# Performance work log

Hardware: AMD Instinct MI355X
Metric: run time of the kernel (lower is better)

The kernel has to match this reference:

```python
import jax, jax.numpy as jnp
import numpy as np

B, T, D, UNITS = 32, 2048, 512, 512


def setup_inputs() -> dict:
    key = jax.random.key(0)
    ks = jax.random.split(key, 8)
    s_d = 1.0 / np.sqrt(D)
    s_u = 1.0 / np.sqrt(UNITS)
    return {
        "features": jax.random.normal(ks[0], (B, T, D), jnp.float32),
        "hidden": jax.random.normal(ks[1], (B, D), jnp.float32),
        "W1": jax.random.normal(ks[2], (D, UNITS), jnp.float32) * s_d,
        "b1": jnp.zeros((UNITS,), jnp.float32),
        "W2": jax.random.normal(ks[3], (D, UNITS), jnp.float32) * s_d,
        "b2": jnp.zeros((UNITS,), jnp.float32),
        "V": jax.random.normal(ks[4], (UNITS, 1), jnp.float32) * s_u,
        "bv": jnp.zeros((1,), jnp.float32),
    }


def reference(features, hidden, W1, b1, W2, b2, V, bv):
    # features: [B,T,D], hidden: [B,D]
    proj_f = jnp.einsum('btd,du->btu', features, W1) + b1      # [B,T,U]
    proj_h = (hidden @ W2 + b2)[:, None, :]                    # [B,1,U]
    score = jnp.tanh(proj_f + proj_h)                          # [B,T,U]
    logits = jnp.einsum('btu,uo->bto', score, V) + bv          # [B,T,1]
    attn = jax.nn.softmax(logits, axis=1)                      # softmax over time
    context = jnp.sum(attn * features, axis=1)                 # [B,D]
    return context, attn
```

## Files before the change

### kernel.cpp

```cpp
#include <hip/hip_runtime.h>
#include <hip/hip_bf16.h>

typedef __bf16 bf16x8 __attribute__((ext_vector_type(8)));
typedef float  float4v __attribute__((ext_vector_type(4)));
typedef unsigned short u16;
typedef u16 u16x8 __attribute__((ext_vector_type(8)));

#define NB 32
#define NT 2048
#define ND 512
#define NU 512
#define BK 64

__device__ __forceinline__ u16 f2bf(float f) {
    union { float f; unsigned u; } v; v.f = f;
    unsigned u = v.u;
    return (u16)((u + 0x7fffu + ((u >> 16) & 1u)) >> 16);
}

__device__ __forceinline__ u16x8 cvt8(float4v a, float4v b) {
    union { __hip_bfloat162 h[4]; u16x8 v; } u;
    u.h[0] = __float22bfloat162_rn(make_float2(a[0], a[1]));
    u.h[1] = __float22bfloat162_rn(make_float2(a[2], a[3]));
    u.h[2] = __float22bfloat162_rn(make_float2(b[0], b[1]));
    u.h[3] = __float22bfloat162_rn(make_float2(b[2], b[3]));
    return u.v;
}

__device__ __forceinline__ float fast_tanh(float x) {
    float e = __expf(-2.f * x);
    return 2.f / (1.f + e) - 1.f;
}

__global__ void k_setup(const float* __restrict__ W1, u16* __restrict__ w1t,
                        const float* __restrict__ hidden, const float* __restrict__ W2,
                        const float* __restrict__ b2, float* __restrict__ projh,
                        float* __restrict__ ctx) {
    __shared__ u16 tile[32][33];
    __shared__ float h[ND];
    __shared__ float part[4][64];
    if (threadIdx.x < 32) ctx[blockIdx.x * 32 + threadIdx.x] = 0.f;

    if (blockIdx.x < 256) {
        int bd = (blockIdx.x & 15) * 32;
        int bu = (blockIdx.x >> 4) * 32;
        int tx = threadIdx.x & 31, ty = threadIdx.x >> 5;
        #pragma unroll
        for (int i = 0; i < 4; ++i)
            tile[ty + i * 8][tx] = f2bf(W1[(bd + ty + i * 8) * NU + bu + tx]);
        __syncthreads();
        #pragma unroll
        for (int i = 0; i < 4; ++i)
            w1t[(bu + ty + i * 8) * ND + bd + tx] = tile[tx][ty + i * 8];
    } else {
        int blk = blockIdx.x - 256;
        int b  = blk >> 3;
        int uc = (blk & 7) * 64;
        int ui = threadIdx.x & 63;
        int du = threadIdx.x >> 6;
        for (int i = threadIdx.x; i < ND; i += 256) h[i] = hidden[b * ND + i];
        __syncthreads();
        int u = uc + ui;
        float acc = 0.f;
        int d0 = du * 128;
        #pragma unroll 8
        for (int d = 0; d < 128; ++d) acc += h[d0 + d] * W2[(d0 + d) * NU + u];
        part[du][ui] = acc;
        __syncthreads();
        if (threadIdx.x < 64)
            projh[b * NU + u] = part[0][ui] + part[1][ui] + part[2][ui] + part[3][ui] + b2[u];
    }
}

__global__ __launch_bounds__(512, 4)
void k_logits(const float* __restrict__ feat, const u16* __restrict__ w1t,
              const float* __restrict__ b1, const float* __restrict__ projh,
              const float* __restrict__ V, float* __restrict__ logits) {
    __shared__ __align__(16) u16 aT[64 * BK];
    __shared__ __align__(16) u16 bT[512 * BK];

    const int row0 = blockIdx.x * 64;
    const int b    = row0 >> 11;
    const int tid  = threadIdx.x;
    const int wave = tid >> 6, lane = tid & 63;
    const int quad = lane >> 4, col = lane & 15;

    float4v acc[4][4];
    #pragma unroll
    for (int mt = 0; mt < 4; ++mt)
        #pragma unroll
        for (int nt = 0; nt < 4; ++nt) acc[mt][nt] = (float4v)0.f;

    const int r_a = tid >> 3, c_a = tid & 7;
    const int wc_a = c_a ^ (r_a & 7);
    const float* agp = feat + (long)row0 * ND + r_a * ND + c_a * 8;

    float4v f0 = *(const float4v*)agp;
    float4v f1 = *(const float4v*)(agp + 4);

    for (int p = 0; p < 8; ++p) {
        const int k0 = p * BK;
        #pragma unroll
        for (int j = 0; j < 8; ++j) {
            int s  = j * 512 + tid;
            int r  = s >> 3;
            int gc = (s & 7) ^ (r & 7);
            const u16* gp = w1t + r * ND + k0 + gc * 8;
            u16* lp = &bT[(j * 512 + wave * 64) * 8];
            __builtin_amdgcn_global_load_lds(
                (const __attribute__((address_space(1))) unsigned int*)gp,
                (__attribute__((address_space(3))) unsigned int*)lp, 16, 0, 0);
        }
        *(u16x8*)(&aT[r_a * BK + wc_a * 8]) = cvt8(f0, f1);
        __syncthreads();
        if (p < 7) {
            const float* gp = agp + (p + 1) * BK;
            f0 = *(const float4v*)gp;
            f1 = *(const float4v*)(gp + 4);
        }
        #pragma unroll
        for (int ks = 0; ks < 2; ++ks) {
            bf16x8 af[4], bf[4];
            #pragma unroll
            for (int mt = 0; mt < 4; ++mt) {
                int ra = mt * 16 + col;
                af[mt] = *(const bf16x8*)(&aT[ra * BK + (((ks * 4 + quad) ^ (ra & 7)) * 8)]);
            }
            #pragma unroll
            for (int nt = 0; nt < 4; ++nt) {
                int rb = wave * 64 + nt * 16 + col;
                bf[nt] = *(const bf16x8*)(&bT[rb * BK + (((ks * 4 + quad) ^ (rb & 7)) * 8)]);
            }
            #pragma unroll
            for (int nt = 0; nt < 4; ++nt)
                #pragma unroll
                for (int mt = 0; mt < 4; ++mt)
                    acc[mt][nt] = __builtin_amdgcn_mfma_f32_16x16x32_bf16(af[mt], bf[nt], acc[mt][nt], 0, 0, 0);
        }
        __syncthreads();
    }

    float b1v[4], phv[4], Vv[4];
    #pragma unroll
    for (int nt = 0; nt < 4; ++nt) {
        int u = wave * 64 + nt * 16 + col;
        b1v[nt] = b1[u];
        phv[nt] = projh[b * NU + u];
        Vv[nt]  = V[u];
    }
    float (*partial)[64] = (float(*)[64])aT;
    #pragma unroll
    for (int mt = 0; mt < 4; ++mt) {
        #pragma unroll
        for (int rg = 0; rg < 4; ++rg) {
            float s = 0.f;
            #pragma unroll
            for (int nt = 0; nt < 4; ++nt) {
                float pv = acc[mt][nt][rg] + b1v[nt] + phv[nt];
                s += fast_tanh(pv) * Vv[nt];
            }
            s += __shfl_xor(s, 1);
            s += __shfl_xor(s, 2);
            s += __shfl_xor(s, 4);
            s += __shfl_xor(s, 8);
            if (col == 0) partial[wave][mt * 16 + quad * 4 + rg] = s;
        }
    }
    __syncthreads();
    if (tid < 64) {
        float v = 0.f;
        #pragma unroll
        for (int w = 0; w < 8; ++w) v += partial[w][tid];
        logits[row0 + tid] = v;
    }
}

__global__ __launch_bounds__(256)
void k_ctxsm(const float* __restrict__ feat, const float* __restrict__ logits,
             float* __restrict__ attn, float* __restrict__ ctx) {
    __shared__ float wm[4], ws[4];
    __shared__ float als[64];
    __shared__ float4v part[128];
    const int b  = blockIdx.x >> 5;
    const int tc = blockIdx.x & 31;
    const int t0 = tc * 64;
    const int tid = threadIdx.x;
    const int lane = tid & 63, wave = tid >> 6;
    const float* lg = logits + b * NT;

    float4v l0 = *(const float4v*)(lg + tid * 8);
    float4v l1 = *(const float4v*)(lg + tid * 8 + 4);
    float m = fmaxf(fmaxf(fmaxf(l0[0], l0[1]), fmaxf(l0[2], l0[3])),
                    fmaxf(fmaxf(l1[0], l1[1]), fmaxf(l1[2], l1[3])));
    for (int o = 1; o < 64; o <<= 1) m = fmaxf(m, __shfl_xor(m, o));
    if (lane == 0) wm[wave] = m;
    __syncthreads();
    m = fmaxf(fmaxf(wm[0], wm[1]), fmaxf(wm[2], wm[3]));
    float s = 0.f;
    #pragma unroll
    for (int i = 0; i < 4; ++i) s += __expf(l0[i] - m);
    #pragma unroll
    for (int i = 0; i < 4; ++i) s += __expf(l1[i] - m);
    for (int o = 1; o < 64; o <<= 1) s += __shfl_xor(s, o);
    if (lane == 0) ws[wave] = s;
    __syncthreads();
    const float inv = 1.f / (ws[0] + ws[1] + ws[2] + ws[3]);

    if (tid < 64) {
        float a = __expf(lg[t0 + tid] - m) * inv;
        als[tid] = a;
        attn[b * NT + t0 + tid] = a;
    }
    __syncthreads();

    const int di = tid & 127, tg = tid >> 7;
    const float* fb = feat + ((long)b * NT + t0 + tg * 32) * ND + di * 4;
    float4v acc = (float4v)0.f;
    #pragma unroll 8
    for (int t = 0; t < 32; ++t) {
        float a = als[tg * 32 + t];
        float4v fv = *(const float4v*)(fb + (long)t * ND);
        acc += a * fv;
    }
    if (tg) part[di] = acc;
    __syncthreads();
    if (!tg) {
        acc += part[di];
        float* cp = &ctx[b * ND + di * 4];
        atomicAdd(cp + 0, acc[0]);
        atomicAdd(cp + 1, acc[1]);
        atomicAdd(cp + 2, acc[2]);
        atomicAdd(cp + 3, acc[3]);
    }
}

extern "C" void kernel_launch(void* const* d_in, const int* in_sizes, int n_in,
                              void* d_out, int out_size, void* d_ws, size_t ws_size,
                              hipStream_t stream) {
    const float* feat   = (const float*)d_in[0];
    const float* hidden = (const float*)d_in[1];
    const float* W1     = (const float*)d_in[2];
    const float* b1     = (const float*)d_in[3];
    const float* W2     = (const float*)d_in[4];
    const float* b2     = (const float*)d_in[5];
    const float* V      = (const float*)d_in[6];

    float* out_ctx  = (float*)d_out;
    float* out_attn = (float*)d_out + NB * ND;

    u16*   w1t    = (u16*)d_ws;
    float* projh  = (float*)((char*)d_ws + 512 * 1024);
    float* logits = (float*)((char*)d_ws + 512 * 1024 + 64 * 1024);

    k_setup <<<512, 256, 0, stream>>>(W1, w1t, hidden, W2, b2, projh, out_ctx);
    k_logits<<<1024, 512, 0, stream>>>(feat, w1t, b1, projh, V, logits);
    k_ctxsm <<<1024, 256, 0, stream>>>(feat, logits, out_attn, out_ctx);
}
```

Measured before the change: 259.0 us.

## Fuse softmax-weighted context into logits kernel using unnormalized exp sums

```diff
diff --git a/kernel.cpp b/kernel.cpp
--- a/kernel.cpp
+++ b/kernel.cpp
@@ -35,11 +35,13 @@
 __global__ void k_setup(const float* __restrict__ W1, u16* __restrict__ w1t,
                         const float* __restrict__ hidden, const float* __restrict__ W2,
                         const float* __restrict__ b2, float* __restrict__ projh,
-                        float* __restrict__ ctx) {
+                        float* __restrict__ ctx_raw, float* __restrict__ Ssum) {
     __shared__ u16 tile[32][33];
     __shared__ float h[ND];
     __shared__ float part[4][64];
-    if (threadIdx.x < 32) ctx[blockIdx.x * 32 + threadIdx.x] = 0.f;
+    if (threadIdx.x < 32) ctx_raw[blockIdx.x * 32 + threadIdx.x] = 0.f;
+    if (blockIdx.x == 0 && threadIdx.x >= 32 && threadIdx.x < 64)
+        Ssum[threadIdx.x - 32] = 0.f;
 
     if (blockIdx.x < 256) {
         int bd = (blockIdx.x & 15) * 32;
@@ -75,7 +77,8 @@
 __global__ __launch_bounds__(512, 4)
 void k_logits(const float* __restrict__ feat, const u16* __restrict__ w1t,
               const float* __restrict__ b1, const float* __restrict__ projh,
-              const float* __restrict__ V, float* __restrict__ logits) {
+              const float* __restrict__ V, float* __restrict__ logits,
+              float* __restrict__ ctx_raw, float* __restrict__ Ssum) {
     __shared__ __align__(16) u16 aT[64 * BK];
     __shared__ __align__(16) u16 bT[512 * BK];
 
@@ -148,7 +151,9 @@
         phv[nt] = projh[b * NU + u];
         Vv[nt]  = V[u];
     }
-    float (*partial)[64] = (float(*)[64])aT;
+    float* fscr = (float*)aT;
+    float (*partial)[64] = (float(*)[64])fscr;
+    float* pw = fscr + 512;
     #pragma unroll
     for (int mt = 0; mt < 4; ++mt) {
         #pragma unroll
@@ -172,65 +177,36 @@
         #pragma unroll
         for (int w = 0; w < 8; ++w) v += partial[w][tid];
         logits[row0 + tid] = v;
-    }
-}
-
-__global__ __launch_bounds__(256)
-void k_ctxsm(const float* __restrict__ feat, const float* __restrict__ logits,
-             float* __restrict__ attn, float* __restrict__ ctx) {
-    __shared__ float wm[4], ws[4];
-    __shared__ float als[64];
-    __shared__ float4v part[128];
-    const int b  = blockIdx.x >> 5;
-    const int tc = blockIdx.x & 31;
-    const int t0 = tc * 64;
-    const int tid = threadIdx.x;
-    const int lane = tid & 63, wave = tid >> 6;
-    const float* lg = logits + b * NT;
-
-    float4v l0 = *(const float4v*)(lg + tid * 8);
-    float4v l1 = *(const float4v*)(lg + tid * 8 + 4);
-    float m = fmaxf(fmaxf(fmaxf(l0[0], l0[1]), fmaxf(l0[2], l0[3])),
-                    fmaxf(fmaxf(l1[0], l1[1]), fmaxf(l1[2], l1[3])));
-    for (int o = 1; o < 64; o <<= 1) m = fmaxf(m, __shfl_xor(m, o));
-    if (lane == 0) wm[wave] = m;
+        float pe = __expf(v);
+        pw[tid] = pe;
+        #pragma unroll
+        for (int o = 1; o < 64; o <<= 1) pe += __shfl_xor(pe, o);
+        if (tid == 0) atomicAdd(&Ssum[b], pe);
+    }
     __syncthreads();
-    m = fmaxf(fmaxf(wm[0], wm[1]), fmaxf(wm[2], wm[3]));
-    float s = 0.f;
-    #pragma unroll
-    for (int i = 0; i < 4; ++i) s += __expf(l0[i] - m);
-    #pragma unroll
-    for (int i = 0; i < 4; ++i) s += __expf(l1[i] - m);
-    for (int o = 1; o < 64; o <<= 1) s += __shfl_xor(s, o);
-    if (lane == 0) ws[wave] = s;
-    __syncthreads();
-    const float inv = 1.f / (ws[0] + ws[1] + ws[2] + ws[3]);
-
-    if (tid < 64) {
-        float a = __expf(lg[t0 + tid] - m) * inv;
-        als[tid] = a;
-        attn[b * NT + t0 + tid] = a;
-    }
-    __syncthreads();
-
-    const int di = tid & 127, tg = tid >> 7;
-    const float* fb = feat + ((long)b * NT + t0 + tg * 32) * ND + di * 4;
-    float4v acc = (float4v)0.f;
-    #pragma unroll 8
-    for (int t = 0; t < 32; ++t) {
-        float a = als[tg * 32 + t];
-        float4v fv = *(const float4v*)(fb + (long)t * ND);
-        acc += a * fv;
-    }
-    if (tg) part[di] = acc;
-    __syncthreads();
-    if (!tg) {
-        acc += part[di];
-        float* cp = &ctx[b * ND + di * 4];
-        atomicAdd(cp + 0, acc[0]);
-        atomicAdd(cp + 1, acc[1]);
-        atomicAdd(cp + 2, acc[2]);
-        atomicAdd(cp + 3, acc[3]);
+
+    {
+        const float* fp = feat + (long)row0 * ND + tid;
+        float c0 = 0.f, c1 = 0.f;
+        #pragma unroll 8
+        for (int t = 0; t < 64; t += 2) {
+            c0 += pw[t]     * fp[(long)t * ND];
+            c1 += pw[t + 1] * fp[(long)(t + 1) * ND];
+        }
+        atomicAdd(&ctx_raw[b * ND + tid], c0 + c1);
+    }
+}
+
+__global__ void k_final(const float* __restrict__ logits, const float* __restrict__ ctx_raw,
+                        const float* __restrict__ Ssum, float* __restrict__ ctx,
+                        float* __restrict__ attn) {
+    const int b = blockIdx.x, tid = threadIdx.x;
+    const float invS = 1.f / Ssum[b];
+    ctx[b * ND + tid] = ctx_raw[b * ND + tid] * invS;
+    #pragma unroll
+    for (int i = 0; i < 4; ++i) {
+        int t = tid + i * 512;
+        attn[b * NT + t] = __expf(logits[b * NT + t]) * invS;
     }
 }
 
@@ -248,11 +224,13 @@
     float* out_ctx  = (float*)d_out;
     float* out_attn = (float*)d_out + NB * ND;
 
-    u16*   w1t    = (u16*)d_ws;
-    float* projh  = (float*)((char*)d_ws + 512 * 1024);
-    float* logits = (float*)((char*)d_ws + 512 * 1024 + 64 * 1024);
-
-    k_setup <<<512, 256, 0, stream>>>(W1, w1t, hidden, W2, b2, projh, out_ctx);
-    k_logits<<<1024, 512, 0, stream>>>(feat, w1t, b1, projh, V, logits);
-    k_ctxsm <<<1024, 256, 0, stream>>>(feat, logits, out_attn, out_ctx);
-}
+    u16*   w1t     = (u16*)d_ws;
+    float* projh   = (float*)((char*)d_ws + 512 * 1024);
+    float* logits  = (float*)((char*)d_ws + 576 * 1024);
+    float* ctx_raw = (float*)((char*)d_ws + 832 * 1024);
+    float* Ssum    = (float*)((char*)d_ws + 896 * 1024);
+
+    k_setup <<<512, 256, 0, stream>>>(W1, w1t, hidden, W2, b2, projh, ctx_raw, Ssum);
+    k_logits<<<1024, 512, 0, stream>>>(feat, w1t, b1, projh, V, logits, ctx_raw, Ssum);
+    k_final <<<NB, 512, 0, stream>>>(logits, ctx_raw, Ssum, out_ctx, out_attn);
+}
```

Result: faster. 249.8 us (-3.6%).
